# Optimization experiments

Measured on AMD Instinct MI355X. Metric: run time of the kernel, lower is better.

Reference implementation:

```python
import jax, jax.numpy as jnp
import numpy as np

N = 12288
IN_DIM = 128
OUT_DIM = 128
LR_SLOPE = 0.01
NEG_INF = -9e16


def setup_inputs() -> dict:
    key = jax.random.key(0)
    k1, k2, k3, k4 = jax.random.split(key, 4)
    emb_mat = jax.random.normal(k1, (N, IN_DIM), dtype=jnp.float32)
    adj_mat = jax.random.randint(k2, (N, N), 0, 2, dtype=jnp.int32)
    # xavier-normal-ish init for params
    W = jax.random.normal(k3, (OUT_DIM, IN_DIM), dtype=jnp.float32) * (2.0 / (IN_DIM + OUT_DIM)) ** 0.5
    a = jax.random.normal(k4, (2 * OUT_DIM, 1), dtype=jnp.float32) * (2.0 / (2 * OUT_DIM + 1)) ** 0.5
    return {"emb_mat": emb_mat, "adj_mat": adj_mat, "W": W, "a": a}


def reference(emb_mat, adj_mat, W, a):
    out_dim = W.shape[0]
    e_new = emb_mat @ W.T                       # [N, D_out]
    a1 = a[:out_dim, :]                         # [D_out, 1]
    a2 = a[out_dim:, :]                         # [D_out, 1]
    source_scores = e_new @ a1                  # [N, 1]
    target_scores = e_new @ a2                  # [N, 1]
    e = source_scores + target_scores.T         # [N, N] outer sum
    e = jax.nn.leaky_relu(e, negative_slope=LR_SLOPE)
    e = jnp.where(adj_mat > 0, e, NEG_INF)
    attention = jax.nn.softmax(e, axis=-1)      # [N, N]
    e_transf = attention @ e_new                # [N, D_out]
    return jax.nn.relu(e_transf)
```

## Files before the change

### kernel.cpp

```cpp
#include <hip/hip_runtime.h>


#define NN 12288
#define DIM 128
#define CSPLIT 16
#define COLS_PER (NN / CSPLIT)

typedef __bf16 bf16x8 __attribute__((ext_vector_type(8)));
typedef float f32x4 __attribute__((ext_vector_type(4)));

__global__ __launch_bounds__(256) void k1_gemm(const float* __restrict__ emb,
                                               const float* __restrict__ W,
                                               const float* __restrict__ a,
                                               __bf16* __restrict__ Vt,
                                               float* __restrict__ s,
                                               float* __restrict__ t) {
  const int lane = threadIdx.x & 63;
  const int wave = threadIdx.x >> 6;
  const int m = lane & 15;
  const int quad = lane >> 4;
  const int row0 = blockIdx.x * 64 + wave * 16;

  f32x4 acc[8];
#pragma unroll
  for (int nb = 0; nb < 8; nb++) acc[nb] = (f32x4){0.f, 0.f, 0.f, 0.f};

#pragma unroll
  for (int ks = 0; ks < 4; ks++) {
    const int k0 = ks * 32 + quad * 8;
    const float* ep = emb + (size_t)(row0 + m) * DIM + k0;
    float4 lo = *(const float4*)ep;
    float4 hi = *(const float4*)(ep + 4);
    bf16x8 af = {(__bf16)lo.x, (__bf16)lo.y, (__bf16)lo.z, (__bf16)lo.w,
                 (__bf16)hi.x, (__bf16)hi.y, (__bf16)hi.z, (__bf16)hi.w};
#pragma unroll
    for (int nb = 0; nb < 8; nb++) {
      const float* wp = W + (size_t)(nb * 16 + m) * DIM + k0;
      float4 wlo = *(const float4*)wp;
      float4 whi = *(const float4*)(wp + 4);
      bf16x8 bf = {(__bf16)wlo.x, (__bf16)wlo.y, (__bf16)wlo.z, (__bf16)wlo.w,
                   (__bf16)whi.x, (__bf16)whi.y, (__bf16)whi.z, (__bf16)whi.w};
      acc[nb] = __builtin_amdgcn_mfma_f32_16x16x32_bf16(af, bf, acc[nb], 0, 0, 0);
    }
  }

  float a1v[8], a2v[8];
#pragma unroll
  for (int nb = 0; nb < 8; nb++) {
    a1v[nb] = a[nb * 16 + m];
    a2v[nb] = a[DIM + nb * 16 + m];
  }
#pragma unroll
  for (int r = 0; r < 4; r++) {
    const int gr = row0 + quad * 4 + r;
    float ps = 0.f, pt = 0.f;
#pragma unroll
    for (int nb = 0; nb < 8; nb++) {
      float e = acc[nb][r];
      ps += e * a1v[nb];
      pt += e * a2v[nb];
      Vt[(size_t)(nb * 16 + m) * NN + gr] = (__bf16)e;
    }
    ps += __shfl_xor(ps, 1); ps += __shfl_xor(ps, 2);
    ps += __shfl_xor(ps, 4); ps += __shfl_xor(ps, 8);
    pt += __shfl_xor(pt, 1); pt += __shfl_xor(pt, 2);
    pt += __shfl_xor(pt, 4); pt += __shfl_xor(pt, 8);
    if (m == 0) { s[gr] = ps; t[gr] = pt; }
  }
}

__global__ __launch_bounds__(256) void ktmax(const float* __restrict__ t,
                                             float* __restrict__ tmax) {
  __shared__ float red[256];
  float mx = -1e30f;
  for (int i = threadIdx.x; i < NN; i += 256) mx = fmaxf(mx, t[i]);
  red[threadIdx.x] = mx;
  __syncthreads();
  for (int off = 128; off; off >>= 1) {
    if ((int)threadIdx.x < off) red[threadIdx.x] = fmaxf(red[threadIdx.x], red[threadIdx.x + off]);
    __syncthreads();
  }
  if (threadIdx.x == 0) *tmax = red[0];
}

__global__ __launch_bounds__(256, 3) void k2_attn(const int* __restrict__ adj,
                                                  const __bf16* __restrict__ Vt,
                                                  const float* __restrict__ s,
                                                  const float* __restrict__ t,
                                                  const float* __restrict__ tmaxp,
                                                  float* __restrict__ part,
                                                  float* __restrict__ lpart) {
  const int lane = threadIdx.x & 63;
  const int wave = threadIdx.x >> 6;
  const int m = lane & 15;
  const int quad = lane >> 4;
  const int row0 = blockIdx.x * 128 + wave * 32;
  const int cs = blockIdx.y;
  const int col0 = cs * COLS_PER;
  const int rowA = row0 + m;
  const int rowB = rowA + 16;

  const float Tmax = *tmaxp;
  const float sA = s[rowA], sB = s[rowB];
  const float uA = sA + Tmax, uB = sB + Tmax;
  const float mA = fmaxf(uA, 0.01f * uA);
  const float mB = fmaxf(uB, 0.01f * uB);

  const int* adjA = adj + (size_t)rowA * NN + col0 + quad * 8;
  const int* adjB = adj + (size_t)rowB * NN + col0 + quad * 8;
  const float* tp = t + col0 + quad * 8;
  const __bf16* vp = Vt + (size_t)m * NN + col0 + quad * 8;

  f32x4 accA[8], accB[8];
#pragma unroll
  for (int nb = 0; nb < 8; nb++) {
    accA[nb] = (f32x4){0.f, 0.f, 0.f, 0.f};
    accB[nb] = (f32x4){0.f, 0.f, 0.f, 0.f};
  }
  float lA = 0.f, lB = 0.f;

  const int iters = COLS_PER / 32;
  int4 cA0 = *(const int4*)(adjA);
  int4 cA1 = *(const int4*)(adjA + 4);
  int4 cB0 = *(const int4*)(adjB);
  int4 cB1 = *(const int4*)(adjB + 4);
  float4 ct0 = *(const float4*)(tp);
  float4 ct1 = *(const float4*)(tp + 4);

  for (int it = 0; it < iters; ++it) {
    const int kb = it * 32;
    const int nkb = (it + 1 < iters) ? kb + 32 : kb;
    int4 nA0 = *(const int4*)(adjA + nkb);
    int4 nA1 = *(const int4*)(adjA + nkb + 4);
    int4 nB0 = *(const int4*)(adjB + nkb);
    int4 nB1 = *(const int4*)(adjB + nkb + 4);
    float4 nt0 = *(const float4*)(tp + nkb);
    float4 nt1 = *(const float4*)(tp + nkb + 4);

    bf16x8 bv[8];
#pragma unroll
    for (int nb = 0; nb < 8; nb++)
      bv[nb] = *(const bf16x8*)(vp + (size_t)nb * 16 * NN + kb);

    bf16x8 pA, pB;
#define PEL(frag, jj, tv, av, ss, mm, ll)                               \
    {                                                                   \
      float v = (ss) + (tv);                                            \
      float lv = fmaxf(v, 0.01f * v);                                   \
      float e = ((av) != 0) ? __expf(lv - (mm)) : 0.f;                  \
      (ll) += e;                                                        \
      frag[jj] = (__bf16)e;                                             \
    }
    PEL(pA, 0, ct0.x, cA0.x, sA, mA, lA)
    PEL(pA, 1, ct0.y, cA0.y, sA, mA, lA)
    PEL(pA, 2, ct0.z, cA0.z, sA, mA, lA)
    PEL(pA, 3, ct0.w, cA0.w, sA, mA, lA)
    PEL(pA, 4, ct1.x, cA1.x, sA, mA, lA)
    PEL(pA, 5, ct1.y, cA1.y, sA, mA, lA)
    PEL(pA, 6, ct1.z, cA1.z, sA, mA, lA)
    PEL(pA, 7, ct1.w, cA1.w, sA, mA, lA)
    PEL(pB, 0, ct0.x, cB0.x, sB, mB, lB)
    PEL(pB, 1, ct0.y, cB0.y, sB, mB, lB)
    PEL(pB, 2, ct0.z, cB0.z, sB, mB, lB)
    PEL(pB, 3, ct0.w, cB0.w, sB, mB, lB)
    PEL(pB, 4, ct1.x, cB1.x, sB, mB, lB)
    PEL(pB, 5, ct1.y, cB1.y, sB, mB, lB)
    PEL(pB, 6, ct1.z, cB1.z, sB, mB, lB)
    PEL(pB, 7, ct1.w, cB1.w, sB, mB, lB)
#undef PEL

#pragma unroll
    for (int nb = 0; nb < 8; nb++) {
      accA[nb] = __builtin_amdgcn_mfma_f32_16x16x32_bf16(pA, bv[nb], accA[nb], 0, 0, 0);
      accB[nb] = __builtin_amdgcn_mfma_f32_16x16x32_bf16(pB, bv[nb], accB[nb], 0, 0, 0);
    }

    cA0 = nA0; cA1 = nA1; cB0 = nB0; cB1 = nB1;
    ct0 = nt0; ct1 = nt1;
  }

  lA += __shfl_xor(lA, 16); lA += __shfl_xor(lA, 32);
  lB += __shfl_xor(lB, 16); lB += __shfl_xor(lB, 32);
  if (quad == 0) {
    lpart[(size_t)cs * NN + rowA] = lA;
    lpart[(size_t)cs * NN + rowB] = lB;
  }

  float* po = part + ((size_t)cs * NN + row0) * DIM;
#pragma unroll
  for (int nb = 0; nb < 8; nb++) {
#pragma unroll
    for (int r = 0; r < 4; r++) {
      po[(size_t)(quad * 4 + r) * DIM + nb * 16 + m] = accA[nb][r];
      po[(size_t)(16 + quad * 4 + r) * DIM + nb * 16 + m] = accB[nb][r];
    }
  }
}

__global__ __launch_bounds__(256) void kl(const float* __restrict__ lpart,
                                          float* __restrict__ linv) {
  const int r = blockIdx.x * 256 + threadIdx.x;
  float l = 0.f;
#pragma unroll
  for (int cs = 0; cs < CSPLIT; cs++) l += lpart[(size_t)cs * NN + r];
  linv[r] = 1.0f / l;
}

__global__ __launch_bounds__(256) void k3_fin(const float* __restrict__ part,
                                              const float* __restrict__ linv,
                                              float* __restrict__ out) {
  const int idx = blockIdx.x * 256 + threadIdx.x;
  const int row = idx >> 5;
  const float4* p4 = (const float4*)part;
  float4 acc = p4[idx];
#pragma unroll
  for (int cs = 1; cs < CSPLIT; cs++) {
    float4 v = p4[(size_t)cs * (NN * DIM / 4) + idx];
    acc.x += v.x; acc.y += v.y; acc.z += v.z; acc.w += v.w;
  }
  const float li = linv[row];
  float4 o;
  o.x = fmaxf(acc.x * li, 0.f);
  o.y = fmaxf(acc.y * li, 0.f);
  o.z = fmaxf(acc.z * li, 0.f);
  o.w = fmaxf(acc.w * li, 0.f);
  ((float4*)out)[idx] = o;
}

extern "C" void kernel_launch(void* const* d_in, const int* in_sizes, int n_in,
                              void* d_out, int out_size, void* d_ws, size_t ws_size,
                              hipStream_t stream) {
  (void)in_sizes; (void)n_in; (void)out_size; (void)ws_size;
  const float* emb = (const float*)d_in[0];
  const int* adj = (const int*)d_in[1];
  const float* W = (const float*)d_in[2];
  const float* a = (const float*)d_in[3];
  float* out = (float*)d_out;

  char* ws = (char*)d_ws;
  __bf16* Vt = (__bf16*)ws;
  float* s = (float*)(ws + 3145728);
  float* t = (float*)(ws + 3194880);
  float* lpart = (float*)(ws + 3244032);
  float* linv = (float*)(ws + 4030464);
  float* tmax = (float*)(ws + 4079616);
  float* part = (float*)(ws + 4079872);

  k1_gemm<<<NN / 64, 256, 0, stream>>>(emb, W, a, Vt, s, t);
  ktmax<<<1, 256, 0, stream>>>(t, tmax);
  dim3 g2(NN / 128, CSPLIT);
  k2_attn<<<g2, 256, 0, stream>>>(adj, Vt, s, t, tmax, part, lpart);
  kl<<<NN / 256, 256, 0, stream>>>(lpart, linv);
  k3_fin<<<NN * DIM / 4 / 256, 256, 0, stream>>>(part, linv, out);
}
```

Measured before the change: 1.011 ms.

## Stage adjacency bytes and V tiles in double-buffered shared memory, halve column split

The attention kernel now loads each 128x32 adjacency tile and the matching V^T tile cooperatively with coalesced loads, packs the adjacency into bytes, and double-buffers both in LDS with one barrier per chunk. Waves then read the mask and V fragments from shared memory instead of each issuing its own strided global loads. The column split drops from 16 to 8, which halves the partial-output writes and the final reduction work but also halves the number of blocks. The cost is LDS traffic and a __syncthreads per 32-column step.

```diff
diff --git a/kernel.cpp b/kernel.cpp
--- a/kernel.cpp
+++ b/kernel.cpp
@@ -3,8 +3,10 @@
 
 #define NN 12288
 #define DIM 128
-#define CSPLIT 16
+#define CSPLIT 8
 #define COLS_PER (NN / CSPLIT)
+#define BK 32
+#define NCHUNK (COLS_PER / BK)
 
 typedef __bf16 bf16x8 __attribute__((ext_vector_type(8)));
 typedef float f32x4 __attribute__((ext_vector_type(4)));
@@ -90,14 +92,18 @@
                                                   const float* __restrict__ tmaxp,
                                                   float* __restrict__ part,
                                                   float* __restrict__ lpart) {
-  const int lane = threadIdx.x & 63;
-  const int wave = threadIdx.x >> 6;
+  __shared__ unsigned long long adjb[2][128][5];
+  __shared__ __attribute__((aligned(16))) __bf16 vtb[2][128][40];
+
+  const int tid = threadIdx.x;
+  const int lane = tid & 63;
+  const int wave = tid >> 6;
   const int m = lane & 15;
   const int quad = lane >> 4;
-  const int row0 = blockIdx.x * 128 + wave * 32;
+  const int row0 = blockIdx.x * 128;
   const int cs = blockIdx.y;
   const int col0 = cs * COLS_PER;
-  const int rowA = row0 + m;
+  const int rowA = row0 + wave * 32 + m;
   const int rowB = rowA + 16;
 
   const float Tmax = *tmaxp;
@@ -106,11 +112,6 @@
   const float mA = fmaxf(uA, 0.01f * uA);
   const float mB = fmaxf(uB, 0.01f * uB);
 
-  const int* adjA = adj + (size_t)rowA * NN + col0 + quad * 8;
-  const int* adjB = adj + (size_t)rowB * NN + col0 + quad * 8;
-  const float* tp = t + col0 + quad * 8;
-  const __bf16* vp = Vt + (size_t)m * NN + col0 + quad * 8;
-
   f32x4 accA[8], accB[8];
 #pragma unroll
   for (int nb = 0; nb < 8; nb++) {
@@ -119,64 +120,82 @@
   }
   float lA = 0.f, lB = 0.f;
 
-  const int iters = COLS_PER / 32;
-  int4 cA0 = *(const int4*)(adjA);
-  int4 cA1 = *(const int4*)(adjA + 4);
-  int4 cB0 = *(const int4*)(adjB);
-  int4 cB1 = *(const int4*)(adjB + 4);
-  float4 ct0 = *(const float4*)(tp);
-  float4 ct1 = *(const float4*)(tp + 4);
-
-  for (int it = 0; it < iters; ++it) {
-    const int kb = it * 32;
-    const int nkb = (it + 1 < iters) ? kb + 32 : kb;
-    int4 nA0 = *(const int4*)(adjA + nkb);
-    int4 nA1 = *(const int4*)(adjA + nkb + 4);
-    int4 nB0 = *(const int4*)(adjB + nkb);
-    int4 nB1 = *(const int4*)(adjB + nkb + 4);
-    float4 nt0 = *(const float4*)(tp + nkb);
-    float4 nt1 = *(const float4*)(tp + nkb + 4);
-
-    bf16x8 bv[8];
-#pragma unroll
-    for (int nb = 0; nb < 8; nb++)
-      bv[nb] = *(const bf16x8*)(vp + (size_t)nb * 16 * NN + kb);
+  int4 ga[4];
+  bf16x8 gv[2];
+  const int fr = tid >> 3, fc = (tid & 7) * 4;
+  const int vd = tid >> 2, vc = (tid & 3) * 8;
+
+  auto fetch = [&](int c) {
+    const int cc = col0 + c * BK;
+#pragma unroll
+    for (int p = 0; p < 4; p++)
+      ga[p] = *(const int4*)(adj + (size_t)(row0 + fr + p * 32) * NN + cc + fc);
+#pragma unroll
+    for (int p = 0; p < 2; p++)
+      gv[p] = *(const bf16x8*)(Vt + (size_t)(vd + p * 64) * NN + cc + vc);
+  };
+  auto commit = [&](int b) {
+#pragma unroll
+    for (int p = 0; p < 4; p++) {
+      unsigned pk = (unsigned)(ga[p].x != 0) | ((unsigned)(ga[p].y != 0) << 8) |
+                    ((unsigned)(ga[p].z != 0) << 16) | ((unsigned)(ga[p].w != 0) << 24);
+      *(unsigned*)((unsigned char*)&adjb[b][fr + p * 32][0] + fc) = pk;
+    }
+#pragma unroll
+    for (int p = 0; p < 2; p++)
+      *(bf16x8*)&vtb[b][vd + p * 64][vc] = gv[p];
+  };
+
+  fetch(0);
+  commit(0);
+  __syncthreads();
+
+  for (int c = 0; c < NCHUNK; c++) {
+    if (c + 1 < NCHUNK) fetch(c + 1);
+
+    const int b = c & 1;
+    const float* tp = t + col0 + c * BK + quad * 8;
+    float4 ct0 = *(const float4*)tp;
+    float4 ct1 = *(const float4*)(tp + 4);
+    unsigned long long avA = adjb[b][wave * 32 + m][quad];
+    unsigned long long avB = adjb[b][wave * 32 + 16 + m][quad];
 
     bf16x8 pA, pB;
 #define PEL(frag, jj, tv, av, ss, mm, ll)                               \
     {                                                                   \
       float v = (ss) + (tv);                                            \
       float lv = fmaxf(v, 0.01f * v);                                   \
-      float e = ((av) != 0) ? __expf(lv - (mm)) : 0.f;                  \
+      float e = (((av) >> (8 * (jj))) & 1) ? __expf(lv - (mm)) : 0.f;   \
       (ll) += e;                                                        \
       frag[jj] = (__bf16)e;                                             \
     }
-    PEL(pA, 0, ct0.x, cA0.x, sA, mA, lA)
-    PEL(pA, 1, ct0.y, cA0.y, sA, mA, lA)
-    PEL(pA, 2, ct0.z, cA0.z, sA, mA, lA)
-    PEL(pA, 3, ct0.w, cA0.w, sA, mA, lA)
-    PEL(pA, 4, ct1.x, cA1.x, sA, mA, lA)
-    PEL(pA, 5, ct1.y, cA1.y, sA, mA, lA)
-    PEL(pA, 6, ct1.z, cA1.z, sA, mA, lA)
-    PEL(pA, 7, ct1.w, cA1.w, sA, mA, lA)
-    PEL(pB, 0, ct0.x, cB0.x, sB, mB, lB)
-    PEL(pB, 1, ct0.y, cB0.y, sB, mB, lB)
-    PEL(pB, 2, ct0.z, cB0.z, sB, mB, lB)
-    PEL(pB, 3, ct0.w, cB0.w, sB, mB, lB)
-    PEL(pB, 4, ct1.x, cB1.x, sB, mB, lB)
-    PEL(pB, 5, ct1.y, cB1.y, sB, mB, lB)
-    PEL(pB, 6, ct1.z, cB1.z, sB, mB, lB)
-    PEL(pB, 7, ct1.w, cB1.w, sB, mB, lB)
+    PEL(pA, 0, ct0.x, avA, sA, mA, lA)
+    PEL(pA, 1, ct0.y, avA, sA, mA, lA)
+    PEL(pA, 2, ct0.z, avA, sA, mA, lA)
+    PEL(pA, 3, ct0.w, avA, sA, mA, lA)
+    PEL(pA, 4, ct1.x, avA, sA, mA, lA)
+    PEL(pA, 5, ct1.y, avA, sA, mA, lA)
+    PEL(pA, 6, ct1.z, avA, sA, mA, lA)
+    PEL(pA, 7, ct1.w, avA, sA, mA, lA)
+    PEL(pB, 0, ct0.x, avB, sB, mB, lB)
+    PEL(pB, 1, ct0.y, avB, sB, mB, lB)
+    PEL(pB, 2, ct0.z, avB, sB, mB, lB)
+    PEL(pB, 3, ct0.w, avB, sB, mB, lB)
+    PEL(pB, 4, ct1.x, avB, sB, mB, lB)
+    PEL(pB, 5, ct1.y, avB, sB, mB, lB)
+    PEL(pB, 6, ct1.z, avB, sB, mB, lB)
+    PEL(pB, 7, ct1.w, avB, sB, mB, lB)
 #undef PEL
 
 #pragma unroll
     for (int nb = 0; nb < 8; nb++) {
-      accA[nb] = __builtin_amdgcn_mfma_f32_16x16x32_bf16(pA, bv[nb], accA[nb], 0, 0, 0);
-      accB[nb] = __builtin_amdgcn_mfma_f32_16x16x32_bf16(pB, bv[nb], accB[nb], 0, 0, 0);
-    }
-
-    cA0 = nA0; cA1 = nA1; cB0 = nB0; cB1 = nB1;
-    ct0 = nt0; ct1 = nt1;
+      bf16x8 bv = *(const bf16x8*)&vtb[b][nb * 16 + m][quad * 8];
+      accA[nb] = __builtin_amdgcn_mfma_f32_16x16x32_bf16(pA, bv, accA[nb], 0, 0, 0);
+      accB[nb] = __builtin_amdgcn_mfma_f32_16x16x32_bf16(pB, bv, accB[nb], 0, 0, 0);
+    }
+
+    if (c + 1 < NCHUNK) commit((c + 1) & 1);
+    __syncthreads();
   }
 
   lA += __shfl_xor(lA, 16); lA += __shfl_xor(lA, 32);
@@ -186,7 +205,7 @@
     lpart[(size_t)cs * NN + rowB] = lB;
   }
 
-  float* po = part + ((size_t)cs * NN + row0) * DIM;
+  float* po = part + ((size_t)cs * NN + row0 + wave * 32) * DIM;
 #pragma unroll
   for (int nb = 0; nb < 8; nb++) {
 #pragma unroll
@@ -242,9 +261,9 @@
   float* s = (float*)(ws + 3145728);
   float* t = (float*)(ws + 3194880);
   float* lpart = (float*)(ws + 3244032);
-  float* linv = (float*)(ws + 4030464);
-  float* tmax = (float*)(ws + 4079616);
-  float* part = (float*)(ws + 4079872);
+  float* linv = (float*)(ws + 3637248);
+  float* tmax = (float*)(ws + 3686400);
+  float* part = (float*)(ws + 3686656);
 
   k1_gemm<<<NN / 64, 256, 0, stream>>>(emb, W, a, Vt, s, t);
   ktmax<<<1, 256, 0, stream>>>(t, tmax);
```

Measured after the change: 823.3 us. 1.23x faster.
